# Optimization experiments

Hardware: AMD Instinct MI355X
Metric: run time of the kernel (lower is better)

Reference implementation:

```python
import jax, jax.numpy as jnp
import numpy as np

TEMPERATURE = 0.1
NUM_POS = 2


def _cross_entropy(logits, labels):
    # mean over batch of -log_softmax(logits)[i, labels[i]]
    logp = jax.nn.log_softmax(logits, axis=-1)
    return -jnp.take_along_axis(logp, labels[:, None], axis=1).mean()


def setup_inputs() -> dict:
    key = jax.random.key(0)
    k1, k2, k3 = jax.random.split(key, 3)
    B, D, Q = 4096, 256, 65536
    embedding = jax.random.normal(k1, (B, D), dtype=jnp.float32)
    preds = jax.random.normal(k2, (B, D), dtype=jnp.float32)
    queue = jax.random.normal(k3, (Q, D), dtype=jnp.float32)
    queue = queue / jnp.linalg.norm(queue, axis=1, keepdims=True)
    return {"embedding": embedding, "preds": preds, "queue": queue}


def reference(embedding, preds, queue):
    B = embedding.shape[0]
    half = B // NUM_POS
    labels = jnp.arange(half)  # single-trainer: dist_rank = 0

    # nearest-neighbor retrieval from the support queue (no-grad in original)
    sim = embedding @ queue.T                      # [B, Q]
    nearest = queue[jnp.argmax(sim, axis=1)]       # [B, D]

    nn_a, nn_b = nearest[:half], nearest[half:]
    preds_a, preds_b = preds[:half], preds[half:]

    logits_ab = (nn_a @ preds_b.T) / TEMPERATURE   # [half, half]
    logits_ba = (nn_b @ preds_a.T) / TEMPERATURE

    loss = _cross_entropy(logits_ab, labels) / 2 + _cross_entropy(logits_ba, labels) / 2
    return loss
```

## Files before the change

kernel.cpp:

```cpp
#include <hip/hip_runtime.h>
#include <hip/hip_bf16.h>
#include <stdint.h>

#define B_ROWS 4096
#define D_K    256
#define Q_ROWS 65536
#define HALF   2048

typedef __bf16 bf16x8 __attribute__((ext_vector_type(8)));
typedef float  f32x4  __attribute__((ext_vector_type(4)));
typedef int    v8i    __attribute__((ext_vector_type(8)));
typedef int    v4i    __attribute__((ext_vector_type(4)));
typedef unsigned short u16x8 __attribute__((ext_vector_type(8)));
typedef const __attribute__((address_space(1))) void* gptr1;
typedef __attribute__((address_space(3))) void* lptr3;

__device__ __forceinline__ unsigned int f32_ordered(float f) {
    unsigned int u = __float_as_uint(f);
    return (u & 0x80000000u) ? ~u : (u | 0x80000000u);
}

__device__ __forceinline__ unsigned short f2bf_rn(float f) {
    unsigned int u = __float_as_uint(f);
    u += 0x7FFFu + ((u >> 16) & 1u);
    return (unsigned short)(u >> 16);
}

#define EMB4  (B_ROWS * D_K / 4)
#define PRED4 (B_ROWS * D_K / 4)
#define QUE4  (Q_ROWS * D_K / 4)
__global__ __launch_bounds__(256) void prep_kernel(const float* __restrict__ emb,
                                                   const float* __restrict__ preds,
                                                   const float* __restrict__ queue,
                                                   unsigned char* __restrict__ emb8,
                                                   unsigned short* __restrict__ preds_bf,
                                                   unsigned char* __restrict__ queue8,
                                                   unsigned long long* __restrict__ amax,
                                                   float* __restrict__ out) {
    int i = blockIdx.x * 256 + threadIdx.x;
    if (i < EMB4) {
        float4 v = ((const float4*)emb)[i];
        int u = __builtin_amdgcn_cvt_pk_fp8_f32(v.x, v.y, 0, false);
        u     = __builtin_amdgcn_cvt_pk_fp8_f32(v.z, v.w, u, true);
        ((int*)emb8)[i] = u;
    } else if (i < EMB4 + PRED4) {
        int off = i - EMB4;
        float4 v = ((const float4*)preds)[off];
        ushort4 o;
        o.x = f2bf_rn(v.x); o.y = f2bf_rn(v.y); o.z = f2bf_rn(v.z); o.w = f2bf_rn(v.w);
        ((ushort4*)preds_bf)[off] = o;
    } else {
        int off = i - EMB4 - PRED4;
        float4 v = ((const float4*)queue)[off];
        int u = __builtin_amdgcn_cvt_pk_fp8_f32(v.x, v.y, 0, false);
        u     = __builtin_amdgcn_cvt_pk_fp8_f32(v.z, v.w, u, true);
        ((int*)queue8)[off] = u;
    }
    if (i < B_ROWS) amax[i] = 0ull;
    if (i == 0) out[0] = 0.f;
}

#define BM 128
#define BN 128
#define NCHUNK 8
#define MFMA_FP8(av, bv, c) \
    __builtin_amdgcn_mfma_scale_f32_16x16x128_f8f6f4((av), (bv), (c), 0, 0, 0, 0x7F7F7F7F, 0, 0x7F7F7F7F)

__global__ __launch_bounds__(256, 2) void sim_argmax_kernel(const unsigned char* __restrict__ A8,
                                                            const unsigned char* __restrict__ B8,
                                                            unsigned long long* __restrict__ amax) {
    __shared__ unsigned char sh[32768];

    const int tid  = threadIdx.x;
    const int wave = tid >> 6;
    const int lane = tid & 63;
    const int l15  = lane & 15;
    const int quad = lane >> 4;

    const int bid  = blockIdx.x;
    const int xcd  = bid & 7;
    const int j    = bid >> 3;
    const int blk_m = (j & 31) * BM;
    const int ngrp  = (j >> 5) * 8 + xcd;
    const int nbase = ngrp * (BN * NCHUNK);

    const int wave_m = (wave >> 1) * 64;
    const int wave_n = (wave & 1) * 64;

    {
        const unsigned char* gA = A8 + (size_t)(blk_m + (tid >> 4)) * D_K
                                     + (((tid & 15) ^ ((tid >> 4) & 15)) << 4);
#pragma unroll
        for (int jj = 0; jj < 8; jj++)
            __builtin_amdgcn_global_load_lds((gptr1)(gA + jj * 4096),
                                             (lptr3)&sh[jj * 4096 + wave * 1024], 16, 0, 0);
    }
    __syncthreads();

    const int pA = (quad * 2) ^ l15;
    v8i areg[2][4];
#pragma unroll
    for (int kt = 0; kt < 2; kt++) {
#pragma unroll
        for (int mi = 0; mi < 4; mi++) {
            const int _lo = (wave_m + mi * 16 + l15) * 256 + ((pA ^ (kt << 3)) << 4);
            v4i _x = *(const v4i*)&sh[_lo];
            v4i _y = *(const v4i*)&sh[_lo ^ 16];
            areg[kt][mi] = __builtin_shufflevector(_x, _y, 0, 1, 2, 3, 4, 5, 6, 7);
        }
    }
    __syncthreads();

    const unsigned char* gB = B8 + (size_t)(nbase + (tid >> 3)) * D_K
                                 + (((tid & 7) ^ ((tid >> 3) & 7)) << 4);

#define PREFB(T, BSOFF) do {                                                           \
        const int _off = ((T) >> 1) * (32 * D_K * 4) + ((T) & 1) * 128;                \
        _Pragma("unroll")                                                              \
        for (int _j = 0; _j < 4; _j++)                                                 \
            __builtin_amdgcn_global_load_lds((gptr1)(gB + _j * 8192 + _off),           \
                                             (lptr3)&sh[(BSOFF) + _j * 4096 + wave * 1024], 16, 0, 0); \
    } while (0)

    int Bbase[4];
#pragma unroll
    for (int ni = 0; ni < 4; ni++) Bbase[ni] = (wave_n + ni * 16 + l15) * 128;
    const int pB = (quad * 2) ^ (l15 & 7);

    float bestv[4][4];
    int   bestc[4][4];
#pragma unroll
    for (int mi = 0; mi < 4; mi++)
#pragma unroll
        for (int reg = 0; reg < 4; reg++) { bestv[mi][reg] = -1e30f; bestc[mi][reg] = 0; }

    f32x4 acc[4][4];
#pragma unroll
    for (int i = 0; i < 4; i++)
#pragma unroll
        for (int jj = 0; jj < 4; jj++) acc[i][jj] = (f32x4){0.f, 0.f, 0.f, 0.f};

#define COMPUTE(BSOFF, KT) do {                                                        \
        _Pragma("unroll")                                                              \
        for (int ni = 0; ni < 4; ni++) {                                               \
            const int _lo = (BSOFF) + Bbase[ni] + (pB << 4);                           \
            v4i _x = *(const v4i*)&sh[_lo];                                            \
            v4i _y = *(const v4i*)&sh[_lo ^ 16];                                       \
            v8i bv = __builtin_shufflevector(_x, _y, 0, 1, 2, 3, 4, 5, 6, 7);          \
            _Pragma("unroll")                                                          \
            for (int mi = 0; mi < 4; mi++)                                             \
                acc[mi][ni] = MFMA_FP8(areg[KT][mi], bv, acc[mi][ni]);                 \
        }                                                                              \
    } while (0)

    PREFB(0, 0);

#pragma unroll 1
    for (int p = 0; p < NCHUNK; ++p) {
        __syncthreads();
        PREFB(2 * p + 1, 16384);
        COMPUTE(0, 0);
        __syncthreads();
        if (p < NCHUNK - 1) PREFB(2 * p + 2, 0);
        COMPUTE(16384, 1);

        const int col0 = nbase + p * BN + wave_n + l15;
#pragma unroll
        for (int mi = 0; mi < 4; mi++) {
#pragma unroll
            for (int reg = 0; reg < 4; reg++) {
#pragma unroll
                for (int ni = 0; ni < 4; ni++) {
                    float v = acc[mi][ni][reg];
                    int   c = col0 + ni * 16;
                    if (v > bestv[mi][reg]) { bestv[mi][reg] = v; bestc[mi][reg] = c; }
                }
                acc[mi][0][reg] = 0.f; acc[mi][1][reg] = 0.f;
                acc[mi][2][reg] = 0.f; acc[mi][3][reg] = 0.f;
            }
        }
    }

#pragma unroll
    for (int mi = 0; mi < 4; mi++) {
#pragma unroll
        for (int reg = 0; reg < 4; reg++) {
            unsigned long long key =
                ((unsigned long long)f32_ordered(bestv[mi][reg]) << 32) |
                (unsigned long long)(0xFFFFFFFFu - (unsigned)bestc[mi][reg]);
#pragma unroll
            for (int m = 1; m < 16; m <<= 1) {
                unsigned long long o = __shfl_xor(key, m, 16);
                if (o > key) key = o;
            }
            if (l15 == mi * 4 + reg) {
                int row = blk_m + wave_m + mi * 16 + quad * 4 + reg;
                atomicMax(&amax[row], key);
            }
        }
    }
}

__global__ __launch_bounds__(512) void logits_ce_kernel(const unsigned long long* __restrict__ amax,
                                                        const float* __restrict__ queue_f32,
                                                        const unsigned short* __restrict__ preds_bf,
                                                        float* __restrict__ out) {
    const int gw   = blockIdx.x;
    const int tid  = threadIdx.x;
    const int wave = tid >> 6;
    const int lane = tid & 63;
    const int l15  = lane & 15;
    const int quad = lane >> 4;
    const int h    = gw >> 7;
    const int rowbase = gw * 16;
    const unsigned short* Bbase = preds_bf + (size_t)((1 - h) * HALF) * D_K;

    __shared__ float sm[8][16], sl[8][16], sd[8][16];

    unsigned idx = 0xFFFFFFFFu - (unsigned)(amax[rowbase + l15] & 0xFFFFFFFFull);
    const float* arow = queue_f32 + (size_t)idx * D_K;
    bf16x8 a[8];
#pragma unroll
    for (int kc = 0; kc < 8; kc++) {
        float4 f0 = *(const float4*)(arow + kc * 32 + quad * 8);
        float4 f1 = *(const float4*)(arow + kc * 32 + quad * 8 + 4);
        u16x8 t;
        t[0] = f2bf_rn(f0.x); t[1] = f2bf_rn(f0.y); t[2] = f2bf_rn(f0.z); t[3] = f2bf_rn(f0.w);
        t[4] = f2bf_rn(f1.x); t[5] = f2bf_rn(f1.y); t[6] = f2bf_rn(f1.z); t[7] = f2bf_rn(f1.w);
        a[kc] = *(const bf16x8*)&t;
    }

    float m_run[4], l_run[4], diag[4];
#pragma unroll
    for (int r = 0; r < 4; r++) { m_run[r] = -1e30f; l_run[r] = 0.f; diag[r] = -1e30f; }

    const int tdiag = gw & 127;
    for (int tt = 0; tt < 16; tt++) {
        const int t = wave * 16 + tt;
        f32x4 acc = (f32x4){0.f, 0.f, 0.f, 0.f};
#pragma unroll
        for (int kc = 0; kc < 8; kc++) {
            bf16x8 b = *(const bf16x8*)&Bbase[(size_t)(t * 16 + l15) * D_K + kc * 32 + quad * 8];
            acc = __builtin_amdgcn_mfma_f32_16x16x32_bf16(a[kc], b, acc, 0, 0, 0);
        }
#pragma unroll
        for (int reg = 0; reg < 4; reg++) {
            float v = acc[reg] * 10.0f;
            if (t == tdiag && l15 == quad * 4 + reg) diag[reg] = v;
            float nm = fmaxf(m_run[reg], v);
            l_run[reg] = l_run[reg] * __expf(m_run[reg] - nm) + __expf(v - nm);
            m_run[reg] = nm;
        }
    }
#pragma unroll
    for (int reg = 0; reg < 4; reg++) {
#pragma unroll
        for (int m = 1; m < 16; m <<= 1) {
            float om = __shfl_xor(m_run[reg], m, 16);
            float ol = __shfl_xor(l_run[reg], m, 16);
            float od = __shfl_xor(diag[reg], m, 16);
            float nm = fmaxf(m_run[reg], om);
            l_run[reg] = l_run[reg] * __expf(m_run[reg] - nm) + ol * __expf(om - nm);
            m_run[reg] = nm;
            diag[reg] = fmaxf(diag[reg], od);
        }
        if (l15 == 0) {
            sm[wave][quad * 4 + reg] = m_run[reg];
            sl[wave][quad * 4 + reg] = l_run[reg];
            sd[wave][quad * 4 + reg] = diag[reg];
        }
    }
    __syncthreads();
    if (tid < 16) {
        float M = -1e30f, L = 0.f, Dg = -1e30f;
#pragma unroll
        for (int w = 0; w < 8; w++) {
            float mw = sm[w][tid], lw = sl[w][tid], dw = sd[w][tid];
            float nM = fmaxf(M, mw);
            L = L * __expf(M - nM) + lw * __expf(mw - nM);
            M = nM;
            Dg = fmaxf(Dg, dw);
        }
        float rl = (M + __logf(L)) - Dg;
#pragma unroll
        for (int m = 1; m < 16; m <<= 1) rl += __shfl_xor(rl, m, 16);
        if (tid == 0) atomicAdd(out, rl * (1.0f / (float)B_ROWS));
    }
}

extern "C" void kernel_launch(void* const* d_in, const int* in_sizes, int n_in,
                              void* d_out, int out_size, void* d_ws, size_t ws_size,
                              hipStream_t stream) {
    const float* emb   = (const float*)d_in[0];
    const float* preds = (const float*)d_in[1];
    const float* queue = (const float*)d_in[2];

    char* w = (char*)d_ws;
    unsigned long long* amax  = (unsigned long long*)w;
    unsigned char*  emb8      = (unsigned char*)(w + (1u << 20));
    unsigned short* preds_bf  = (unsigned short*)(w + (2u << 20));
    unsigned char*  queue8    = (unsigned char*)(w + (4u << 20));

    prep_kernel<<<dim3((EMB4 + PRED4 + QUE4) / 256), 256, 0, stream>>>(
        emb, preds, queue, emb8, preds_bf, queue8, amax, (float*)d_out);
    sim_argmax_kernel<<<dim3((B_ROWS / BM) * (Q_ROWS / (BN * NCHUNK))), 256, 0, stream>>>(
        emb8, queue8, amax);
    logits_ce_kernel<<<dim3(B_ROWS / 16), 512, 0, stream>>>(
        amax, queue, preds_bf, (float*)d_out);
}
```

Baseline: 212.9 us.

## Triple-buffer B tiles and overlap argmax fold with next chunk's MFMAs

Moves the B-tile LDS staging from double to triple buffering, using explicit vmcnt waits and raw barriers so two prefetches can be in flight. It ping-pongs two accumulator sets so the argmax comparison for one chunk runs interleaved with the MFMAs of the next, and zero-initializes through the MFMA instead of explicit clears. It also raises wave priority around MFMA blocks. The cost is more LDS (48KB) and doubled accumulator registers, which could pressure occupancy at 2 blocks per CU.

```diff
diff --git a/kernel.cpp b/kernel.cpp
--- a/kernel.cpp
+++ b/kernel.cpp
@@ -66,10 +66,15 @@
 #define MFMA_FP8(av, bv, c) \
     __builtin_amdgcn_mfma_scale_f32_16x16x128_f8f6f4((av), (bv), (c), 0, 0, 0, 0x7F7F7F7F, 0, 0x7F7F7F7F)
 
+#define WAITV(N) asm volatile("s_waitcnt vmcnt(" #N ")" ::: "memory")
+#define BARRIER() do { __builtin_amdgcn_s_barrier(); \
+                       asm volatile("" ::: "memory"); \
+                       __builtin_amdgcn_sched_barrier(0); } while (0)
+
 __global__ __launch_bounds__(256, 2) void sim_argmax_kernel(const unsigned char* __restrict__ A8,
                                                             const unsigned char* __restrict__ B8,
                                                             unsigned long long* __restrict__ amax) {
-    __shared__ unsigned char sh[32768];
+    __shared__ unsigned char sh[49152];
 
     const int tid  = threadIdx.x;
     const int wave = tid >> 6;
@@ -134,13 +139,11 @@
 #pragma unroll
         for (int reg = 0; reg < 4; reg++) { bestv[mi][reg] = -1e30f; bestc[mi][reg] = 0; }
 
-    f32x4 acc[4][4];
-#pragma unroll
-    for (int i = 0; i < 4; i++)
-#pragma unroll
-        for (int jj = 0; jj < 4; jj++) acc[i][jj] = (f32x4){0.f, 0.f, 0.f, 0.f};
-
-#define COMPUTE(BSOFF, KT) do {                                                        \
+    f32x4 accA[4][4], accB[4][4];
+    const f32x4 zero4 = (f32x4){0.f, 0.f, 0.f, 0.f};
+
+#define COMPUTE0(BSOFF, AC) do {                                                       \
+        __builtin_amdgcn_s_setprio(1);                                                 \
         _Pragma("unroll")                                                              \
         for (int ni = 0; ni < 4; ni++) {                                               \
             const int _lo = (BSOFF) + Bbase[ni] + (pB << 4);                           \
@@ -149,37 +152,73 @@
             v8i bv = __builtin_shufflevector(_x, _y, 0, 1, 2, 3, 4, 5, 6, 7);          \
             _Pragma("unroll")                                                          \
             for (int mi = 0; mi < 4; mi++)                                             \
-                acc[mi][ni] = MFMA_FP8(areg[KT][mi], bv, acc[mi][ni]);                 \
+                AC[mi][ni] = MFMA_FP8(areg[0][mi], bv, zero4);                         \
         }                                                                              \
+        __builtin_amdgcn_s_setprio(0);                                                 \
     } while (0)
 
-    PREFB(0, 0);
+#define COMPUTE1(BSOFF, AC) do {                                                       \
+        __builtin_amdgcn_s_setprio(1);                                                 \
+        _Pragma("unroll")                                                              \
+        for (int ni = 0; ni < 4; ni++) {                                               \
+            const int _lo = (BSOFF) + Bbase[ni] + (pB << 4);                           \
+            v4i _x = *(const v4i*)&sh[_lo];                                            \
+            v4i _y = *(const v4i*)&sh[_lo ^ 16];                                       \
+            v8i bv = __builtin_shufflevector(_x, _y, 0, 1, 2, 3, 4, 5, 6, 7);          \
+            _Pragma("unroll")                                                          \
+            for (int mi = 0; mi < 4; mi++)                                             \
+                AC[mi][ni] = MFMA_FP8(areg[1][mi], bv, AC[mi][ni]);                    \
+        }                                                                              \
+        __builtin_amdgcn_s_setprio(0);                                                 \
+    } while (0)
+
+#define FOLDH(AC, PP, HH) do {                                                         \
+        const int _col0 = nbase + (PP) * BN + wave_n + l15;                            \
+        _Pragma("unroll")                                                              \
+        for (int mi = 2 * (HH); mi < 2 * (HH) + 2; mi++)                               \
+            _Pragma("unroll")                                                          \
+            for (int reg = 0; reg < 4; reg++)                                          \
+                _Pragma("unroll")                                                      \
+                for (int ni = 0; ni < 4; ni++) {                                       \
+                    float v = AC[mi][ni][reg];                                         \
+                    int   c = _col0 + ni * 16;                                         \
+                    if (v > bestv[mi][reg]) { bestv[mi][reg] = v; bestc[mi][reg] = c; }\
+                }                                                                      \
+    } while (0)
+
+#define ROT() do { int _t = b0; b0 = b1; b1 = b2; b2 = _t; } while (0)
+
+    int b0 = 0, b1 = 16384, b2 = 32768;
+
+    PREFB(0, b0);
+    PREFB(1, b1);
 
 #pragma unroll 1
-    for (int p = 0; p < NCHUNK; ++p) {
-        __syncthreads();
-        PREFB(2 * p + 1, 16384);
-        COMPUTE(0, 0);
-        __syncthreads();
-        if (p < NCHUNK - 1) PREFB(2 * p + 2, 0);
-        COMPUTE(16384, 1);
-
-        const int col0 = nbase + p * BN + wave_n + l15;
-#pragma unroll
-        for (int mi = 0; mi < 4; mi++) {
-#pragma unroll
-            for (int reg = 0; reg < 4; reg++) {
-#pragma unroll
-                for (int ni = 0; ni < 4; ni++) {
-                    float v = acc[mi][ni][reg];
-                    int   c = col0 + ni * 16;
-                    if (v > bestv[mi][reg]) { bestv[mi][reg] = v; bestc[mi][reg] = c; }
-                }
-                acc[mi][0][reg] = 0.f; acc[mi][1][reg] = 0.f;
-                acc[mi][2][reg] = 0.f; acc[mi][3][reg] = 0.f;
-            }
-        }
-    }
+    for (int P = 0; P < NCHUNK; P += 2) {
+        WAITV(4); BARRIER();
+        PREFB(2 * P + 2, b2);
+        COMPUTE0(b0, accA);
+        if (P > 0) FOLDH(accB, P - 1, 0);
+        ROT();
+        WAITV(4); BARRIER();
+        PREFB(2 * P + 3, b2);
+        COMPUTE1(b0, accA);
+        if (P > 0) FOLDH(accB, P - 1, 1);
+        ROT();
+        WAITV(4); BARRIER();
+        if (P < NCHUNK - 2) PREFB(2 * P + 4, b2);
+        COMPUTE0(b0, accB);
+        FOLDH(accA, P, 0);
+        ROT();
+        if (P < NCHUNK - 2) { WAITV(4); } else { WAITV(0); }
+        BARRIER();
+        if (P < NCHUNK - 2) PREFB(2 * P + 5, b2);
+        COMPUTE1(b0, accB);
+        FOLDH(accA, P, 1);
+        ROT();
+    }
+    FOLDH(accB, NCHUNK - 1, 0);
+    FOLDH(accB, NCHUNK - 1, 1);
 
 #pragma unroll
     for (int mi = 0; mi < 4; mi++) {
```

Measured after the change: 242.6 us. 13.9% more time.
